# Optimization experiments

Measured on AMD Instinct MI355X. Metric: run time of the kernel, lower is better.

The kernel has to match this reference:

```python
import jax, jax.numpy as jnp
import numpy as np

N = 100000   # nodes (single node type 'word')
R = 4        # relation types (sorted rel_names)
E = 160000   # edges per relation
H = 128      # h_dim
O = 64       # out_dim


def setup_inputs() -> dict:
    key = jax.random.key(0)
    k0, k1, k2, k3 = jax.random.split(key, 4)
    embed = jax.random.normal(k0, (N, H), jnp.float32) * 0.1          # RelGraphEmbed table
    weight = jax.random.normal(k1, (R, H, O), jnp.float32) / np.sqrt(H)  # layer-2 per-rel weight
    bias1 = jnp.zeros((H,), jnp.float32)   # layer-1 h_bias
    bias2 = jnp.zeros((O,), jnp.float32)   # layer-2 h_bias
    edge_src = jax.random.randint(k2, (R, E), 0, N)
    edge_dst = jax.random.randint(k3, (R, E), 0, N)
    return dict(embed=embed, weight=weight, bias1=bias1, bias2=bias2,
                edge_src=edge_src, edge_dst=edge_dst)


def _rel_mean(x, src, dst, num_nodes):
    # GraphConv(norm='right'): sum messages into dst, divide by dst in-degree.
    msg = x[src]                                                    # [E, d] gather
    summed = jax.ops.segment_sum(msg, dst, num_segments=num_nodes)  # scatter-add
    deg = jax.ops.segment_sum(jnp.ones(src.shape, x.dtype), dst, num_segments=num_nodes)
    return summed / jnp.maximum(deg, 1.0)[:, None]


def reference(embed, weight, bias1, bias2, edge_src, edge_dst):
    n = embed.shape[0]
    # Layer 1: weight=False -> HeteroGraphConv sums right-normalized aggregations, then bias+relu.
    h1 = jnp.zeros_like(embed)
    for r in range(edge_src.shape[0]):
        h1 = h1 + _rel_mean(embed, edge_src[r], edge_dst[r], n)
    h1 = jax.nn.relu(h1 + bias1)
    # Layer 2: per-relation linear transform, aggregate, sum over relations, bias (no activation).
    out = jnp.zeros((n, weight.shape[-1]), embed.dtype)
    for r in range(edge_src.shape[0]):
        out = out + _rel_mean(h1 @ weight[r], edge_src[r], edge_dst[r], n)
    return out + bias2
```

## Files before the change

### kernel.cpp

```cpp
#include <hip/hip_runtime.h>
#include <hip/hip_bf16.h>

#define H 128
#define O 64
#define RELS 4

typedef short short8 __attribute__((ext_vector_type(8)));
typedef float f32x4 __attribute__((ext_vector_type(4)));
typedef unsigned int u32x4 __attribute__((ext_vector_type(4)));

static __device__ __forceinline__ unsigned short f2b(float x) {
    __hip_bfloat16 h = __float2bfloat16(x);
    return *reinterpret_cast<unsigned short*>(&h);
}
static __device__ __forceinline__ float blo(unsigned u) { return __uint_as_float(u << 16); }
static __device__ __forceinline__ float bhi(unsigned u) { return __uint_as_float(u & 0xffff0000u); }

#define ACC8(acc, uv, wt)                                           \
    acc[0] += (wt) * blo(uv.x); acc[1] += (wt) * bhi(uv.x);         \
    acc[2] += (wt) * blo(uv.y); acc[3] += (wt) * bhi(uv.y);         \
    acc[4] += (wt) * blo(uv.z); acc[5] += (wt) * bhi(uv.z);         \
    acc[6] += (wt) * blo(uv.w); acc[7] += (wt) * bhi(uv.w);

__global__ void k_prep(const float* __restrict__ embed, unsigned short* __restrict__ eb,
                       const float* __restrict__ W, unsigned short* __restrict__ WT,
                       const int* __restrict__ dst, int* __restrict__ cnt,
                       int n4, int wtot, int E, int RE, int N, int b_h, int b_cvt, int b_tot) {
    for (int b = blockIdx.x; b < b_tot; b += gridDim.x) {
        if (b < b_h) {
            int i = b * 256 + threadIdx.x;
            if (i < RE) { int r = i / E; atomicAdd(&cnt[r * N + dst[i]], 1); }
        } else if (b < b_h + b_cvt) {
            int base = (b - b_h) * 1024;
#pragma unroll
            for (int k = 0; k < 4; ++k) {
                int i = base + k * 256 + threadIdx.x;
                if (i < n4) {
                    f32x4 v = __builtin_nontemporal_load(((const f32x4*)embed) + i);
                    ushort4 o;
                    o.x = f2b(v[0]); o.y = f2b(v[1]); o.z = f2b(v[2]); o.w = f2b(v[3]);
                    ((ushort4*)eb)[i] = o;
                }
            }
        } else {
            int i = (b - b_h - b_cvt) * 256 + threadIdx.x;
            if (i < wtot) {
                int r = i >> 13;
                int n = (i >> 7) & (O - 1);
                int k = i & (H - 1);
                WT[i] = f2b(W[((size_t)r * H + k) * O + n]);
            }
        }
    }
}

__global__ void k_scan1(const int* __restrict__ cnt, int* __restrict__ offs,
                        int* __restrict__ bsum, int n, int N_) {
    __shared__ int sh[256];
    int t = threadIdx.x;
    int base = blockIdx.x * 1024 + t * 4;
    int4 v = make_int4(0, 0, 0, 0);
    if (base + 3 < n && (N_ & 3) == 0) {
#pragma unroll
        for (int r = 0; r < RELS; ++r) {
            int4 c = *(const int4*)(cnt + (size_t)r * N_ + base);
            v.x += c.x; v.y += c.y; v.z += c.z; v.w += c.w;
        }
    } else {
        for (int j = 0; j < 4; ++j) {
            int i = base + j;
            if (i < n) {
                int s = 0;
                for (int r = 0; r < RELS; ++r) s += cnt[(size_t)r * N_ + i];
                (&v.x)[j] = s;
            }
        }
    }
    int s = v.x + v.y + v.z + v.w;
    sh[t] = s; __syncthreads();
    for (int off = 1; off < 256; off <<= 1) {
        int x = (t >= off) ? sh[t - off] : 0;
        __syncthreads();
        sh[t] += x;
        __syncthreads();
    }
    int incl = sh[t];
    int ex = incl - s;
    if (base < n)     offs[base]     = ex;
    if (base + 1 < n) offs[base + 1] = ex + v.x;
    if (base + 2 < n) offs[base + 2] = ex + v.x + v.y;
    if (base + 3 < n) offs[base + 3] = ex + v.x + v.y + v.z;
    if (t == 255) bsum[blockIdx.x] = incl;
}

__global__ void k_scan3c(int* __restrict__ offs, const int* __restrict__ bsum, int nb,
                         const int* __restrict__ cnt, int* __restrict__ cursor,
                         int* __restrict__ ctr, int n, int total, int N_) {
    __shared__ int sb[256];
    int t = threadIdx.x;
    int s = (t < nb) ? bsum[t] : 0;
    sb[t] = s; __syncthreads();
    for (int off = 1; off < 256; off <<= 1) {
        int x = (t >= off) ? sb[t - off] : 0;
        __syncthreads();
        sb[t] += x;
        __syncthreads();
    }
    int ex = sb[t] - s;
    __syncthreads();
    sb[t] = ex;
    __syncthreads();

    int i = blockIdx.x * blockDim.x + t;
    if (i < n) {
        int off = offs[i] + sb[i >> 10];
        offs[i] = off;
        int c0 = cnt[i], c1 = cnt[N_ + i], c2 = cnt[2 * N_ + i];
        cursor[i]          = off;
        cursor[N_ + i]     = off + c0;
        cursor[2 * N_ + i] = off + c0 + c1;
        cursor[3 * N_ + i] = off + c0 + c1 + c2;
    }
    if (i == 0) { offs[n] = total; ctr[0] = 0; }
}

__global__ void k_fill(const int* __restrict__ src, const int* __restrict__ dst,
                       const int* __restrict__ cnt, int* __restrict__ cursor,
                       uint2* __restrict__ ue, int E, int RE, int N) {
    for (int i = blockIdx.x * blockDim.x + threadIdx.x; i < RE; i += gridDim.x * blockDim.x) {
        int r = i / E;
        int d = dst[i];
        int pos = atomicAdd(&cursor[r * N + d], 1);
        float w = 1.0f / (float)max(cnt[r * N + d], 1);
        ue[pos] = make_uint2((unsigned)(r * N + src[i]), __float_as_uint(w));
    }
}

__global__ __launch_bounds__(256) void k_l1g(const unsigned short* __restrict__ eb,
                                             const int* __restrict__ offs2,
                                             const uint2* __restrict__ ue,
                                             const float* __restrict__ bias1,
                                             const unsigned short* __restrict__ WT,
                                             unsigned short* __restrict__ T,
                                             int* __restrict__ ctr,
                                             int N, int ntiles) {
    __shared__ __align__(16) unsigned short hs[2][16][136];
    __shared__ __align__(16) unsigned short st[4][16][72];
    __shared__ int s_tile[2];
    int tid = threadIdx.x, wv = tid >> 6, l = tid & 63;
    int nloc = tid >> 4;
    int q = l & 15;
    int rA = l & 15, kb = (l >> 4) * 8;
    unsigned N1 = (unsigned)N, N2 = (unsigned)(2 * N);

    float4 b0 = *(const float4*)(bias1 + q * 8);
    float4 b1 = *(const float4*)(bias1 + q * 8 + 4);
    const unsigned short* Wb = WT + (size_t)wv * O * H;

    if (tid == 0) s_tile[0] = atomicAdd(ctr, 1);
    __syncthreads();

    int p = 0;
    for (;;) {
        int tile = s_tile[p];
        if (tile >= ntiles) break;
        if (tid == 0) s_tile[p ^ 1] = atomicAdd(ctr, 1);

        int row0 = tile * 16;
        int node = row0 + nloc;

        float a[8] = {0.f, 0.f, 0.f, 0.f, 0.f, 0.f, 0.f, 0.f};
        float c[8] = {0.f, 0.f, 0.f, 0.f, 0.f, 0.f, 0.f, 0.f};
        if (node < N) {
            int2 be = *(const int2*)(offs2 + node);
            int beg = be.x, end = be.y;
            int e = beg;
            for (; e + 4 <= end; e += 4) {
                uint2 p0 = ue[e], p1 = ue[e + 1], p2 = ue[e + 2], p3 = ue[e + 3];
                unsigned s0 = p0.x; if (s0 >= N2) s0 -= N2; if (s0 >= N1) s0 -= N1;
                unsigned s1 = p1.x; if (s1 >= N2) s1 -= N2; if (s1 >= N1) s1 -= N1;
                unsigned s2 = p2.x; if (s2 >= N2) s2 -= N2; if (s2 >= N1) s2 -= N1;
                unsigned s3 = p3.x; if (s3 >= N2) s3 -= N2; if (s3 >= N1) s3 -= N1;
                float w0 = __uint_as_float(p0.y), w1 = __uint_as_float(p1.y);
                float w2 = __uint_as_float(p2.y), w3 = __uint_as_float(p3.y);
                uint4 u0 = *(const uint4*)(eb + (size_t)s0 * H + q * 8);
                uint4 u1 = *(const uint4*)(eb + (size_t)s1 * H + q * 8);
                uint4 u2 = *(const uint4*)(eb + (size_t)s2 * H + q * 8);
                uint4 u3 = *(const uint4*)(eb + (size_t)s3 * H + q * 8);
                ACC8(a, u0, w0);
                ACC8(c, u1, w1);
                ACC8(a, u2, w2);
                ACC8(c, u3, w3);
            }
            for (; e + 2 <= end; e += 2) {
                uint2 p0 = ue[e], p1 = ue[e + 1];
                unsigned s0 = p0.x; if (s0 >= N2) s0 -= N2; if (s0 >= N1) s0 -= N1;
                unsigned s1 = p1.x; if (s1 >= N2) s1 -= N2; if (s1 >= N1) s1 -= N1;
                float w0 = __uint_as_float(p0.y), w1 = __uint_as_float(p1.y);
                uint4 u0 = *(const uint4*)(eb + (size_t)s0 * H + q * 8);
                uint4 u1 = *(const uint4*)(eb + (size_t)s1 * H + q * 8);
                ACC8(a, u0, w0);
                ACC8(c, u1, w1);
            }
            if (e < end) {
                uint2 p0 = ue[e];
                unsigned s0 = p0.x; if (s0 >= N2) s0 -= N2; if (s0 >= N1) s0 -= N1;
                float w0 = __uint_as_float(p0.y);
                uint4 u0 = *(const uint4*)(eb + (size_t)s0 * H + q * 8);
                ACC8(a, u0, w0);
            }
            float f0 = fmaxf(a[0] + c[0] + b0.x, 0.f);
            float f1 = fmaxf(a[1] + c[1] + b0.y, 0.f);
            float f2 = fmaxf(a[2] + c[2] + b0.z, 0.f);
            float f3 = fmaxf(a[3] + c[3] + b0.w, 0.f);
            float f4 = fmaxf(a[4] + c[4] + b1.x, 0.f);
            float f5 = fmaxf(a[5] + c[5] + b1.y, 0.f);
            float f6 = fmaxf(a[6] + c[6] + b1.z, 0.f);
            float f7 = fmaxf(a[7] + c[7] + b1.w, 0.f);
            uint4 o;
            o.x = (unsigned)f2b(f0) | ((unsigned)f2b(f1) << 16);
            o.y = (unsigned)f2b(f2) | ((unsigned)f2b(f3) << 16);
            o.z = (unsigned)f2b(f4) | ((unsigned)f2b(f5) << 16);
            o.w = (unsigned)f2b(f6) | ((unsigned)f2b(f7) << 16);
            *(uint4*)&hs[p][nloc][q * 8] = o;
        } else {
            uint4 zz = make_uint4(0, 0, 0, 0);
            *(uint4*)&hs[p][nloc][q * 8] = zz;
        }
        __syncthreads();

        short8 af[4];
#pragma unroll
        for (int kk = 0; kk < 4; ++kk)
            af[kk] = *(const short8*)&hs[p][rA][kk * 32 + kb];

        f32x4 z = {0.f, 0.f, 0.f, 0.f};
        f32x4 acc[4] = {z, z, z, z};
#pragma unroll
        for (int nt = 0; nt < 4; ++nt) {
            short8 bfr[4];
#pragma unroll
            for (int kk = 0; kk < 4; ++kk)
                bfr[kk] = *(const short8*)(Wb + ((size_t)(nt * 16 + rA)) * H + kk * 32 + kb);
#pragma unroll
            for (int kk = 0; kk < 4; ++kk)
                acc[nt] = __builtin_amdgcn_mfma_f32_16x16x32_bf16(af[kk], bfr[kk], acc[nt], 0, 0, 0);
        }

#pragma unroll
        for (int nt = 0; nt < 4; ++nt)
#pragma unroll
            for (int j = 0; j < 4; ++j)
                st[wv][(l >> 4) * 4 + j][nt * 16 + rA] = f2b(acc[nt][j]);

#pragma unroll
        for (int i = 0; i < 2; ++i) {
            int rr = i * 8 + (l >> 3);
            u32x4 v = *(const u32x4*)&st[wv][rr][(l & 7) * 8];
            int grow = row0 + rr;
            if (grow < N)
                __builtin_nontemporal_store(v, (u32x4*)(T + ((size_t)wv * N + grow) * O + (l & 7) * 8));
        }
        p ^= 1;
    }
}

__global__ void k_pull2(const unsigned short* __restrict__ T, const int* __restrict__ offs2,
                        const uint2* __restrict__ ue, const float* __restrict__ bias2,
                        float* __restrict__ out, int N) {
    int node = blockIdx.x * 32 + (threadIdx.x >> 3);
    if (node >= N) return;
    int o = threadIdx.x & 7;
    int2 be = *(const int2*)(offs2 + node);
    int beg = be.x, end = be.y;

    float a[8] = {0.f, 0.f, 0.f, 0.f, 0.f, 0.f, 0.f, 0.f};
    float c[8] = {0.f, 0.f, 0.f, 0.f, 0.f, 0.f, 0.f, 0.f};

    int e = beg;
    for (; e + 4 <= end; e += 4) {
        uint2 p0 = ue[e], p1 = ue[e + 1], p2 = ue[e + 2], p3 = ue[e + 3];
        float w0 = __uint_as_float(p0.y), w1 = __uint_as_float(p1.y);
        float w2 = __uint_as_float(p2.y), w3 = __uint_as_float(p3.y);
        uint4 u0 = *(const uint4*)(T + (size_t)p0.x * O + o * 8);
        uint4 u1 = *(const uint4*)(T + (size_t)p1.x * O + o * 8);
        uint4 u2 = *(const uint4*)(T + (size_t)p2.x * O + o * 8);
        uint4 u3 = *(const uint4*)(T + (size_t)p3.x * O + o * 8);
        ACC8(a, u0, w0);
        ACC8(c, u1, w1);
        ACC8(a, u2, w2);
        ACC8(c, u3, w3);
    }
    for (; e + 2 <= end; e += 2) {
        uint2 p0 = ue[e], p1 = ue[e + 1];
        float w0 = __uint_as_float(p0.y), w1 = __uint_as_float(p1.y);
        uint4 u0 = *(const uint4*)(T + (size_t)p0.x * O + o * 8);
        uint4 u1 = *(const uint4*)(T + (size_t)p1.x * O + o * 8);
        ACC8(a, u0, w0);
        ACC8(c, u1, w1);
    }
    if (e < end) {
        uint2 p0 = ue[e];
        float w0 = __uint_as_float(p0.y);
        uint4 u0 = *(const uint4*)(T + (size_t)p0.x * O + o * 8);
        ACC8(a, u0, w0);
    }

    float4 b0 = *(const float4*)(bias2 + o * 8);
    float4 b1 = *(const float4*)(bias2 + o * 8 + 4);
    f32x4 v0, v1;
    v0[0] = a[0] + c[0] + b0.x; v0[1] = a[1] + c[1] + b0.y;
    v0[2] = a[2] + c[2] + b0.z; v0[3] = a[3] + c[3] + b0.w;
    v1[0] = a[4] + c[4] + b1.x; v1[1] = a[5] + c[5] + b1.y;
    v1[2] = a[6] + c[6] + b1.z; v1[3] = a[7] + c[7] + b1.w;
    __builtin_nontemporal_store(v0, (f32x4*)(out + (size_t)node * O + o * 8));
    __builtin_nontemporal_store(v1, (f32x4*)(out + (size_t)node * O + o * 8 + 4));
}

extern "C" void kernel_launch(void* const* d_in, const int* in_sizes, int n_in,
                              void* d_out, int out_size, void* d_ws, size_t ws_size,
                              hipStream_t stream) {
    const float* embed  = (const float*)d_in[0];
    const float* weight = (const float*)d_in[1];
    const float* bias1  = (const float*)d_in[2];
    const float* bias2  = (const float*)d_in[3];
    const int*   esrc   = (const int*)d_in[4];
    const int*   edst   = (const int*)d_in[5];
    float* out = (float*)d_out;

    const int N = in_sizes[0] / H;
    const int E = in_sizes[4] / RELS;
    const int RN = RELS * N;
    const int RE = RELS * E;

    char* p = (char*)d_ws;
    auto alloc = [&](size_t bytes) {
        char* q = p;
        p += (bytes + 255) & ~(size_t)255;
        return q;
    };
    int* cnt    = (int*)alloc((size_t)RN * 4);
    int* offs2  = (int*)alloc(((size_t)N + 1) * 4);
    int* cursor = (int*)alloc((size_t)RN * 4);
    int* bsum   = (int*)alloc(4096);
    int* ctr    = (int*)alloc(256);
    uint2* ue   = (uint2*)alloc((size_t)RE * 8);
    unsigned short* eb  = (unsigned short*)alloc((size_t)N * H * 2);
    unsigned short* WT  = (unsigned short*)alloc((size_t)RELS * O * H * 2);
    unsigned short* T   = (unsigned short*)alloc((size_t)RELS * N * O * 2);

    hipMemsetAsync(cnt, 0, (size_t)RN * 4, stream);

    int n4 = N * H / 4;
    int wtot = RELS * O * H;
    int b_h   = (RE + 255) / 256;
    int b_cvt = (n4 + 1023) / 1024;
    int b_w   = (wtot + 255) / 256;
    int b_tot = b_h + b_cvt + b_w;
    int gprep = b_tot < 2048 ? b_tot : 2048;
    k_prep<<<gprep, 256, 0, stream>>>(embed, eb, weight, WT, edst, cnt,
                                      n4, wtot, E, RE, N, b_h, b_cvt, b_tot);

    int nb = (N + 1023) / 1024;
    k_scan1<<<nb, 256, 0, stream>>>(cnt, offs2, bsum, N, N);
    k_scan3c<<<(N + 255) / 256, 256, 0, stream>>>(offs2, bsum, nb, cnt, cursor, ctr, N, RE, N);

    int bfill = (RE + 255) / 256;
    k_fill<<<(bfill < 2048 ? bfill : 2048), 256, 0, stream>>>(esrc, edst, cnt, cursor, ue, E, RE, N);

    int ntiles = (N + 15) / 16;
    k_l1g<<<(ntiles < 2048 ? ntiles : 2048), 256, 0, stream>>>(eb, offs2, ue, bias1, WT, T, ctr, N, ntiles);

    int ngroups = (N + 31) / 32;
    k_pull2<<<ngroups, 256, 0, stream>>>(T, offs2, ue, bias2, out, N);
}
```

Baseline: 210.7 us.

## Edge-balanced layer-1 gather with LDS float atomics and register-resident weights

Layer-1 aggregation now splits each 16-node tile's edge range evenly across 16 thread groups instead of one group per node. Partial sums go into an fp32 LDS tile through shared-memory atomicAdd, using a per-edge local-node byte array written in k_fill. The aim is to remove load imbalance from uneven in-degrees. The layer-2 weight fragments are hoisted into registers once per block, and the atomic work-stealing counter is replaced by a static grid-stride tile schedule with a grid sized to about 1536 blocks. In exchange it adds eight LDS atomics per edge per lane, an extra sync per tile, an extra byte array to write and read, and higher register pressure from holding the weights.

```diff
diff --git a/kernel.cpp b/kernel.cpp
--- a/kernel.cpp
+++ b/kernel.cpp
@@ -95,7 +95,7 @@
 
 __global__ void k_scan3c(int* __restrict__ offs, const int* __restrict__ bsum, int nb,
                          const int* __restrict__ cnt, int* __restrict__ cursor,
-                         int* __restrict__ ctr, int n, int total, int N_) {
+                         int n, int total, int N_) {
     __shared__ int sb[256];
     int t = threadIdx.x;
     int s = (t < nb) ? bsum[t] : 0;
@@ -121,137 +121,119 @@
         cursor[2 * N_ + i] = off + c0 + c1;
         cursor[3 * N_ + i] = off + c0 + c1 + c2;
     }
-    if (i == 0) { offs[n] = total; ctr[0] = 0; }
+    if (i == 0) offs[n] = total;
 }
 
 __global__ void k_fill(const int* __restrict__ src, const int* __restrict__ dst,
                        const int* __restrict__ cnt, int* __restrict__ cursor,
-                       uint2* __restrict__ ue, int E, int RE, int N) {
+                       uint2* __restrict__ ue, unsigned char* __restrict__ unl,
+                       int E, int RE, int N) {
     for (int i = blockIdx.x * blockDim.x + threadIdx.x; i < RE; i += gridDim.x * blockDim.x) {
         int r = i / E;
         int d = dst[i];
         int pos = atomicAdd(&cursor[r * N + d], 1);
         float w = 1.0f / (float)max(cnt[r * N + d], 1);
         ue[pos] = make_uint2((unsigned)(r * N + src[i]), __float_as_uint(w));
+        unl[pos] = (unsigned char)(d & 15);
     }
 }
 
 __global__ __launch_bounds__(256) void k_l1g(const unsigned short* __restrict__ eb,
                                              const int* __restrict__ offs2,
                                              const uint2* __restrict__ ue,
+                                             const unsigned char* __restrict__ unl,
                                              const float* __restrict__ bias1,
                                              const unsigned short* __restrict__ WT,
                                              unsigned short* __restrict__ T,
-                                             int* __restrict__ ctr,
                                              int N, int ntiles) {
-    __shared__ __align__(16) unsigned short hs[2][16][136];
+    __shared__ float ha[2][16][132];
     __shared__ __align__(16) unsigned short st[4][16][72];
-    __shared__ int s_tile[2];
     int tid = threadIdx.x, wv = tid >> 6, l = tid & 63;
-    int nloc = tid >> 4;
-    int q = l & 15;
+    int g = tid >> 4;
+    int q = tid & 15;
     int rA = l & 15, kb = (l >> 4) * 8;
     unsigned N1 = (unsigned)N, N2 = (unsigned)(2 * N);
 
     float4 b0 = *(const float4*)(bias1 + q * 8);
     float4 b1 = *(const float4*)(bias1 + q * 8 + 4);
     const unsigned short* Wb = WT + (size_t)wv * O * H;
-
-    if (tid == 0) s_tile[0] = atomicAdd(ctr, 1);
+    short8 bf[4][4];
+#pragma unroll
+    for (int nt = 0; nt < 4; ++nt)
+#pragma unroll
+        for (int kk = 0; kk < 4; ++kk)
+            bf[nt][kk] = *(const short8*)(Wb + ((size_t)(nt * 16 + rA)) * H + kk * 32 + kb);
+
+    *(float4*)&ha[0][g][q * 8]     = b0;
+    *(float4*)&ha[0][g][q * 8 + 4] = b1;
+    *(float4*)&ha[1][g][q * 8]     = b0;
+    *(float4*)&ha[1][g][q * 8 + 4] = b1;
     __syncthreads();
 
     int p = 0;
-    for (;;) {
-        int tile = s_tile[p];
-        if (tile >= ntiles) break;
-        if (tid == 0) s_tile[p ^ 1] = atomicAdd(ctr, 1);
-
+    for (int tile = blockIdx.x; tile < ntiles; tile += gridDim.x, p ^= 1) {
         int row0 = tile * 16;
-        int node = row0 + nloc;
-
-        float a[8] = {0.f, 0.f, 0.f, 0.f, 0.f, 0.f, 0.f, 0.f};
-        float c[8] = {0.f, 0.f, 0.f, 0.f, 0.f, 0.f, 0.f, 0.f};
-        if (node < N) {
-            int2 be = *(const int2*)(offs2 + node);
-            int beg = be.x, end = be.y;
-            int e = beg;
-            for (; e + 4 <= end; e += 4) {
-                uint2 p0 = ue[e], p1 = ue[e + 1], p2 = ue[e + 2], p3 = ue[e + 3];
-                unsigned s0 = p0.x; if (s0 >= N2) s0 -= N2; if (s0 >= N1) s0 -= N1;
-                unsigned s1 = p1.x; if (s1 >= N2) s1 -= N2; if (s1 >= N1) s1 -= N1;
-                unsigned s2 = p2.x; if (s2 >= N2) s2 -= N2; if (s2 >= N1) s2 -= N1;
-                unsigned s3 = p3.x; if (s3 >= N2) s3 -= N2; if (s3 >= N1) s3 -= N1;
-                float w0 = __uint_as_float(p0.y), w1 = __uint_as_float(p1.y);
-                float w2 = __uint_as_float(p2.y), w3 = __uint_as_float(p3.y);
-                uint4 u0 = *(const uint4*)(eb + (size_t)s0 * H + q * 8);
-                uint4 u1 = *(const uint4*)(eb + (size_t)s1 * H + q * 8);
-                uint4 u2 = *(const uint4*)(eb + (size_t)s2 * H + q * 8);
-                uint4 u3 = *(const uint4*)(eb + (size_t)s3 * H + q * 8);
-                ACC8(a, u0, w0);
-                ACC8(c, u1, w1);
-                ACC8(a, u2, w2);
-                ACC8(c, u3, w3);
-            }
-            for (; e + 2 <= end; e += 2) {
-                uint2 p0 = ue[e], p1 = ue[e + 1];
-                unsigned s0 = p0.x; if (s0 >= N2) s0 -= N2; if (s0 >= N1) s0 -= N1;
-                unsigned s1 = p1.x; if (s1 >= N2) s1 -= N2; if (s1 >= N1) s1 -= N1;
-                float w0 = __uint_as_float(p0.y), w1 = __uint_as_float(p1.y);
-                uint4 u0 = *(const uint4*)(eb + (size_t)s0 * H + q * 8);
-                uint4 u1 = *(const uint4*)(eb + (size_t)s1 * H + q * 8);
-                ACC8(a, u0, w0);
-                ACC8(c, u1, w1);
-            }
-            if (e < end) {
-                uint2 p0 = ue[e];
-                unsigned s0 = p0.x; if (s0 >= N2) s0 -= N2; if (s0 >= N1) s0 -= N1;
-                float w0 = __uint_as_float(p0.y);
-                uint4 u0 = *(const uint4*)(eb + (size_t)s0 * H + q * 8);
-                ACC8(a, u0, w0);
-            }
-            float f0 = fmaxf(a[0] + c[0] + b0.x, 0.f);
-            float f1 = fmaxf(a[1] + c[1] + b0.y, 0.f);
-            float f2 = fmaxf(a[2] + c[2] + b0.z, 0.f);
-            float f3 = fmaxf(a[3] + c[3] + b0.w, 0.f);
-            float f4 = fmaxf(a[4] + c[4] + b1.x, 0.f);
-            float f5 = fmaxf(a[5] + c[5] + b1.y, 0.f);
-            float f6 = fmaxf(a[6] + c[6] + b1.z, 0.f);
-            float f7 = fmaxf(a[7] + c[7] + b1.w, 0.f);
-            uint4 o;
-            o.x = (unsigned)f2b(f0) | ((unsigned)f2b(f1) << 16);
-            o.y = (unsigned)f2b(f2) | ((unsigned)f2b(f3) << 16);
-            o.z = (unsigned)f2b(f4) | ((unsigned)f2b(f5) << 16);
-            o.w = (unsigned)f2b(f6) | ((unsigned)f2b(f7) << 16);
-            *(uint4*)&hs[p][nloc][q * 8] = o;
-        } else {
-            uint4 zz = make_uint4(0, 0, 0, 0);
-            *(uint4*)&hs[p][nloc][q * 8] = zz;
+        int hi = row0 + 16 < N ? row0 + 16 : N;
+        int ebeg = offs2[row0];
+        int eend = offs2[hi];
+        int Et = eend - ebeg;
+        int C = (Et + 15) >> 4;
+        int e0 = ebeg + g * C;
+        int e1 = e0 + C < eend ? e0 + C : eend;
+
+        for (int e = e0; e < e1; ++e) {
+            uint2 pe = ue[e];
+            int nl = unl[e];
+            unsigned s = pe.x; if (s >= N2) s -= N2; if (s >= N1) s -= N1;
+            float w = __uint_as_float(pe.y);
+            uint4 u = *(const uint4*)(eb + (size_t)s * H + q * 8);
+            float* row = &ha[p][nl][q * 8];
+            atomicAdd(row + 0, w * blo(u.x));
+            atomicAdd(row + 1, w * bhi(u.x));
+            atomicAdd(row + 2, w * blo(u.y));
+            atomicAdd(row + 3, w * bhi(u.y));
+            atomicAdd(row + 4, w * blo(u.z));
+            atomicAdd(row + 5, w * bhi(u.z));
+            atomicAdd(row + 6, w * blo(u.w));
+            atomicAdd(row + 7, w * bhi(u.w));
         }
         __syncthreads();
 
         short8 af[4];
 #pragma unroll
-        for (int kk = 0; kk < 4; ++kk)
-            af[kk] = *(const short8*)&hs[p][rA][kk * 32 + kb];
+        for (int kk = 0; kk < 4; ++kk) {
+            f32x4 v0 = *(const f32x4*)&ha[p][rA][kk * 32 + kb];
+            f32x4 v1 = *(const f32x4*)&ha[p][rA][kk * 32 + kb + 4];
+            short8 t;
+            t[0] = (short)f2b(fmaxf(v0[0], 0.f));
+            t[1] = (short)f2b(fmaxf(v0[1], 0.f));
+            t[2] = (short)f2b(fmaxf(v0[2], 0.f));
+            t[3] = (short)f2b(fmaxf(v0[3], 0.f));
+            t[4] = (short)f2b(fmaxf(v1[0], 0.f));
+            t[5] = (short)f2b(fmaxf(v1[1], 0.f));
+            t[6] = (short)f2b(fmaxf(v1[2], 0.f));
+            t[7] = (short)f2b(fmaxf(v1[3], 0.f));
+            af[kk] = t;
+        }
 
         f32x4 z = {0.f, 0.f, 0.f, 0.f};
         f32x4 acc[4] = {z, z, z, z};
 #pragma unroll
-        for (int nt = 0; nt < 4; ++nt) {
-            short8 bfr[4];
+        for (int nt = 0; nt < 4; ++nt)
 #pragma unroll
             for (int kk = 0; kk < 4; ++kk)
-                bfr[kk] = *(const short8*)(Wb + ((size_t)(nt * 16 + rA)) * H + kk * 32 + kb);
-#pragma unroll
-            for (int kk = 0; kk < 4; ++kk)
-                acc[nt] = __builtin_amdgcn_mfma_f32_16x16x32_bf16(af[kk], bfr[kk], acc[nt], 0, 0, 0);
-        }
+                acc[nt] = __builtin_amdgcn_mfma_f32_16x16x32_bf16(af[kk], bf[nt][kk], acc[nt], 0, 0, 0);
 
 #pragma unroll
         for (int nt = 0; nt < 4; ++nt)
 #pragma unroll
             for (int j = 0; j < 4; ++j)
                 st[wv][(l >> 4) * 4 + j][nt * 16 + rA] = f2b(acc[nt][j]);
+
+        __syncthreads();
+
+        *(float4*)&ha[p][g][q * 8]     = b0;
+        *(float4*)&ha[p][g][q * 8 + 4] = b1;
 
 #pragma unroll
         for (int i = 0; i < 2; ++i) {
@@ -261,7 +243,6 @@
             if (grow < N)
                 __builtin_nontemporal_store(v, (u32x4*)(T + ((size_t)wv * N + grow) * O + (l & 7) * 8));
         }
-        p ^= 1;
     }
 }
 
@@ -343,8 +324,8 @@
     int* offs2  = (int*)alloc(((size_t)N + 1) * 4);
     int* cursor = (int*)alloc((size_t)RN * 4);
     int* bsum   = (int*)alloc(4096);
-    int* ctr    = (int*)alloc(256);
     uint2* ue   = (uint2*)alloc((size_t)RE * 8);
+    unsigned char* unl = (unsigned char*)alloc((size_t)RE);
     unsigned short* eb  = (unsigned short*)alloc((size_t)N * H * 2);
     unsigned short* WT  = (unsigned short*)alloc((size_t)RELS * O * H * 2);
     unsigned short* T   = (unsigned short*)alloc((size_t)RELS * N * O * 2);
@@ -363,13 +344,16 @@
 
     int nb = (N + 1023) / 1024;
     k_scan1<<<nb, 256, 0, stream>>>(cnt, offs2, bsum, N, N);
-    k_scan3c<<<(N + 255) / 256, 256, 0, stream>>>(offs2, bsum, nb, cnt, cursor, ctr, N, RE, N);
+    k_scan3c<<<(N + 255) / 256, 256, 0, stream>>>(offs2, bsum, nb, cnt, cursor, N, RE, N);
 
     int bfill = (RE + 255) / 256;
-    k_fill<<<(bfill < 2048 ? bfill : 2048), 256, 0, stream>>>(esrc, edst, cnt, cursor, ue, E, RE, N);
+    k_fill<<<(bfill < 2048 ? bfill : 2048), 256, 0, stream>>>(esrc, edst, cnt, cursor,
+                                                              ue, unl, E, RE, N);
 
     int ntiles = (N + 15) / 16;
-    k_l1g<<<(ntiles < 2048 ? ntiles : 2048), 256, 0, stream>>>(eb, offs2, ue, bias1, WT, T, ctr, N, ntiles);
+    int tpb = (ntiles + 1535) / 1536;
+    int gl1g = (ntiles + tpb - 1) / tpb;
+    k_l1g<<<gl1g, 256, 0, stream>>>(eb, offs2, ue, unl, bias1, WT, T, N, ntiles);
 
     int ngroups = (N + 31) / 32;
     k_pull2<<<ngroups, 256, 0, stream>>>(T, offs2, ue, bias2, out, N);
```

Measured after the change: 561.9 us. 167% more time.
